# Optimization experiments

Hardware: AMD Instinct MI355X
Metric: run time of the kernel (lower is better)

## Reference

```python
import jax, jax.numpy as jnp
import numpy as np

B, M, E, R, U, I = 4096, 100, 128, 64, 100000, 100000


def setup_inputs() -> dict:
    key = jax.random.key(0)
    ks = jax.random.split(key, 10)
    return {
        "user_id": jax.random.randint(ks[0], (B,), 0, U),
        "item_id_p": jax.random.randint(ks[1], (B,), 0, I),
        "item_id_n": jax.random.randint(ks[2], (B,), 0, I),
        "inter_id": jax.random.randint(ks[3], (B, M), 0, I),
        "user_emb_w": jax.random.normal(ks[4], (U, E), jnp.float32),
        "item_emb_w": jax.random.normal(ks[5], (I, E), jnp.float32),
        "ua_key": jax.random.normal(ks[6], (R, E), jnp.float32),
        "ua_val": jax.random.normal(ks[7], (R, E), jnp.float32),
        "ia_key": jax.random.normal(ks[8], (R, E), jnp.float32),
        "ia_val": jax.random.normal(ks[9], (R, E), jnp.float32),
    }


def _maxnorm_lookup(w, ids, max_norm=1.0, eps=1e-7):
    # torch nn.Embedding(max_norm=1): rows with norm > max_norm are renormalized
    v = w[ids]
    n = jnp.linalg.norm(v, axis=-1, keepdims=True)
    scale = jnp.where(n > max_norm, max_norm / (n + eps), jnp.ones_like(n))
    return v * scale


def _rel_attn(key_w, val_w, mul_feat, attn_feat, inter):
    # w = key*val elementwise (R,E); einsum 'mbj,ij->bmj' sums w over relations
    wsum = jnp.sum(key_w * val_w, axis=0)                 # (E,)
    rel = mul_feat[:, None, :] * inter * wsum             # (B,M,E) rel_vecs
    logits = jnp.einsum("bme,be->bm", rel, attn_feat)      # (B,M)
    attn = jax.nn.softmax(logits, axis=1)
    return jnp.einsum("bm,bme->be", attn, rel)             # (B,E)


def reference(user_id, item_id_p, item_id_n, inter_id,
              user_emb_w, item_emb_w, ua_key, ua_val, ia_key, ia_val):
    u = _maxnorm_lookup(user_emb_w, user_id)
    ip = _maxnorm_lookup(item_emb_w, item_id_p)
    inn = _maxnorm_lookup(item_emb_w, item_id_n)
    inter = _maxnorm_lookup(item_emb_w, inter_id)
    # UserAttention: rel from item*inter, softmax vs user
    # ItemAttention (model_type='plus'): rel from user*inter, softmax vs item
    rel_p = _rel_attn(ua_key, ua_val, ip, u, inter) + _rel_attn(ia_key, ia_val, u, ip, inter)
    rel_n = _rel_attn(ua_key, ua_val, inn, u, inter) + _rel_attn(ia_key, ia_val, u, inn, inter)
    return (u, ip, inn, rel_p, rel_n)
```

## Files before the change

kernel.cpp:

```cpp
#include <hip/hip_runtime.h>
#include <math.h>

#define BB 4096
#define MM 100
#define EE 128
#define RR 64

typedef float v4f __attribute__((ext_vector_type(4)));
typedef float v2f __attribute__((ext_vector_type(2)));

__device__ __forceinline__ v4f ld4v(const float* p) {
    return *reinterpret_cast<const v4f*>(p);
}
__device__ __forceinline__ void st4v(float* p, v4f v) {
    *reinterpret_cast<v4f*>(p) = v;
}
__device__ __forceinline__ float pdot8(v4f a, v4f qa, v4f b, v4f qb) {
    v2f acc = a.xy * qa.xy;
    acc += a.zw * qa.zw;
    acc += b.xy * qb.xy;
    acc += b.zw * qb.zw;
    return acc.x + acc.y;
}
__device__ __forceinline__ v4f v4red(v4f a, int off) {
    a.x += __shfl_xor(a.x, off, 64); a.y += __shfl_xor(a.y, off, 64);
    a.z += __shfl_xor(a.z, off, 64); a.w += __shfl_xor(a.w, off, 64);
    return a;
}
__device__ __forceinline__ v4f relcomb(v4f x1, v4f w1, v4f S1v, float i1,
                                       v4f x2, v4f w2, v4f S2v, float i2) {
    return x1 * w1 * (S1v * i1) + x2 * w2 * (S2v * i2);
}

template<int CTRL>
__device__ __forceinline__ float dpp_add(float x) {
    int y = __builtin_amdgcn_update_dpp(0, __float_as_int(x), CTRL, 0xF, 0xF, true);
    return x + __int_as_float(y);
}
__device__ __forceinline__ float row16_allreduce(float x) {
    x = dpp_add<0x121>(x);
    x = dpp_add<0x122>(x);
    x = dpp_add<0x124>(x);
    x = dpp_add<0x128>(x);
    return x;
}

__global__ __launch_bounds__(512)
void wsum_kernel(const float* __restrict__ ua_key, const float* __restrict__ ua_val,
                 const float* __restrict__ ia_key, const float* __restrict__ ia_val,
                 float* __restrict__ ws) {
    __shared__ float part[4][EE];
    const float* k = (blockIdx.x == 0) ? ua_key : ia_key;
    const float* v = (blockIdx.x == 0) ? ua_val : ia_val;
    int e = threadIdx.x & 127;
    int q = threadIdx.x >> 7;
    float s = 0.f;
    #pragma unroll
    for (int j = 0; j < 16; ++j) {
        int r = q * 16 + j;
        s += k[r * EE + e] * v[r * EE + e];
    }
    part[q][e] = s;
    __syncthreads();
    if (threadIdx.x < EE)
        ws[blockIdx.x * EE + e] = part[0][e] + part[1][e] + part[2][e] + part[3][e];
}

__global__ __launch_bounds__(64)
void hlrm_main(const int* __restrict__ user_id,
               const int* __restrict__ ip_id,
               const int* __restrict__ in_id,
               const int* __restrict__ inter_id,
               const float* __restrict__ user_w,
               const float* __restrict__ item_w,
               const float* __restrict__ ws,
               float* __restrict__ out) {
    __shared__ int sw[MM];

    const int b    = blockIdx.x;
    const int lane = threadIdx.x;
    const int g    = lane >> 4;
    const int hl   = lane & 15;
    const int e0   = hl * 4;

    const int* ib = inter_id + b * MM;
    int sid0 = ib[g], sid1 = ib[4 + g], sid2 = ib[8 + g], sid3 = ib[12 + g];
    if (lane < 50)
        *reinterpret_cast<int2*>(sw + 2 * lane) =
            *reinterpret_cast<const int2*>(ib + 2 * lane);

    int uid = user_id[b], pid = ip_id[b], nid = in_id[b];
    const float* pu = user_w + ((uint)uid << 7);
    const float* pp = item_w + ((uint)pid << 7);
    const float* pn = item_w + ((uint)nid << 7);
    v4f ru_a = ld4v(pu + e0), ru_b = ld4v(pu + e0 + 64);
    v4f rp_a = ld4v(pp + e0), rp_b = ld4v(pp + e0 + 64);
    v4f rn_a = ld4v(pn + e0), rn_b = ld4v(pn + e0 + 64);
    v4f waa = ld4v(ws + e0),       wab = ld4v(ws + e0 + 64);
    v4f wia = ld4v(ws + 128 + e0), wib = ld4v(ws + 192 + e0);

    v4f va0, vb0, va1, vb1, va2, vb2, va3, vb3;
#define LOADT(J) do {                                             \
        const float* pt = item_w + ((uint)sid##J << 7) + e0;      \
        va##J = ld4v(pt);                                         \
        vb##J = ld4v(pt + 64);                                    \
    } while (0)
    LOADT(0); LOADT(1); LOADT(2); LOADT(3);

    float ssu = pdot8(ru_a, ru_a, ru_b, ru_b);
    float ssp = pdot8(rp_a, rp_a, rp_b, rp_b);
    float ssn = pdot8(rn_a, rn_a, rn_b, rn_b);
    ssu = row16_allreduce(ssu);
    ssp = row16_allreduce(ssp);
    ssn = row16_allreduce(ssn);
    float scu = (ssu > 1.f) ? __builtin_amdgcn_rsqf(ssu) : 1.f;
    float scp = (ssp > 1.f) ? __builtin_amdgcn_rsqf(ssp) : 1.f;
    float scn = (ssn > 1.f) ? __builtin_amdgcn_rsqf(ssn) : 1.f;

    float cup = scu * scp, cun = scu * scn;
    v4f qa0 = ru_a * rp_a * waa * cup, qb0 = ru_b * rp_b * wab * cup;
    v4f qa1 = ru_a * rp_a * wia * cup, qb1 = ru_b * rp_b * wib * cup;
    v4f qa2 = ru_a * rn_a * waa * cun, qb2 = ru_b * rn_b * wab * cun;
    v4f qa3 = ru_a * rn_a * wia * cun, qb3 = ru_b * rn_b * wib * cun;

    v4f Sa0 = {0,0,0,0}, Sa1 = {0,0,0,0}, Sa2 = {0,0,0,0}, Sa3 = {0,0,0,0};
    v4f Sb0 = {0,0,0,0}, Sb1 = {0,0,0,0}, Sb2 = {0,0,0,0}, Sb3 = {0,0,0,0};
    float den0 = 0.f, den1 = 0.f, den2 = 0.f, den3 = 0.f;

    sid0 = sw[16 + g]; sid1 = sw[20 + g]; sid2 = sw[24 + g]; sid3 = sw[28 + g];

#define STEP(J) do {                                                        \
        float ss = pdot8(va##J, va##J, vb##J, vb##J);                       \
        float d0 = pdot8(va##J, qa0, vb##J, qb0);                           \
        float d1 = pdot8(va##J, qa1, vb##J, qb1);                           \
        float d2 = pdot8(va##J, qa2, vb##J, qb2);                           \
        float d3 = pdot8(va##J, qa3, vb##J, qb3);                           \
        ss = row16_allreduce(ss);                                           \
        d0 = row16_allreduce(d0); d1 = row16_allreduce(d1);                 \
        d2 = row16_allreduce(d2); d3 = row16_allreduce(d3);                 \
        float sc = (ss > 1.f) ? __builtin_amdgcn_rsqf(ss) : 1.f;            \
        float w0 = __expf(d0 * sc), w1 = __expf(d1 * sc);                   \
        float w2 = __expf(d2 * sc), w3 = __expf(d3 * sc);                   \
        den0 += w0; den1 += w1; den2 += w2; den3 += w3;                     \
        w0 *= sc; w1 *= sc; w2 *= sc; w3 *= sc;                             \
        Sa0 += va##J * w0; Sb0 += vb##J * w0;                               \
        Sa1 += va##J * w1; Sb1 += vb##J * w1;                               \
        Sa2 += va##J * w2; Sb2 += vb##J * w2;                               \
        Sa3 += va##J * w3; Sb3 += vb##J * w3;                               \
    } while (0)

    #pragma unroll 1
    for (int it = 0; it < 5; ++it) {
        STEP(0); LOADT(0);
        STEP(1); LOADT(1);
        STEP(2); LOADT(2);
        STEP(3); LOADT(3);
        if (it < 4) {
            int o = 16 * it + 32 + g;
            sid0 = sw[o]; sid1 = sw[o + 4]; sid2 = sw[o + 8]; sid3 = sw[o + 12];
        }
    }
    sid0 = sw[96 + g];
    STEP(0); LOADT(0);
    STEP(1); STEP(2); STEP(3);
    STEP(0);
#undef STEP
#undef LOADT

    #pragma unroll
    for (int off = 16; off < 64; off <<= 1) {
        Sa0 = v4red(Sa0, off); Sb0 = v4red(Sb0, off);
        Sa1 = v4red(Sa1, off); Sb1 = v4red(Sb1, off);
        Sa2 = v4red(Sa2, off); Sb2 = v4red(Sb2, off);
        Sa3 = v4red(Sa3, off); Sb3 = v4red(Sb3, off);
        den0 += __shfl_xor(den0, off, 64);
        den1 += __shfl_xor(den1, off, 64);
        den2 += __shfl_xor(den2, off, 64);
        den3 += __shfl_xor(den3, off, 64);
    }
    float iD0 = 1.f / den0, iD1 = 1.f / den1, iD2 = 1.f / den2, iD3 = 1.f / den3;

    const float* qu = user_w + ((uint)uid << 7);
    const float* qp = item_w + ((uint)pid << 7);
    const float* qn = item_w + ((uint)nid << 7);
    v4f u_a = ld4v(qu + e0) * scu,      u_b = ld4v(qu + e0 + 64) * scu;
    v4f p_a = ld4v(qp + e0) * scp,      p_b = ld4v(qp + e0 + 64) * scp;
    v4f n_a = ld4v(qn + e0) * scn,      n_b = ld4v(qn + e0 + 64) * scn;
    v4f w0a = ld4v(ws + e0),            w0b = ld4v(ws + e0 + 64);
    v4f w1a = ld4v(ws + 128 + e0),      w1b = ld4v(ws + 192 + e0);

    size_t base = (size_t)b * EE;
    const size_t P = (size_t)BB * EE;
    if (g == 0) {
        v4f ra = relcomb(p_a, w0a, Sa0, iD0, u_a, w1a, Sa1, iD1);
        v4f rb = relcomb(p_b, w0b, Sb0, iD0, u_b, w1b, Sb1, iD1);
        st4v(out + 3 * P + base + e0, ra);
        st4v(out + 3 * P + base + e0 + 64, rb);
    } else if (g == 1) {
        v4f ra = relcomb(n_a, w0a, Sa2, iD2, u_a, w1a, Sa3, iD3);
        v4f rb = relcomb(n_b, w0b, Sb2, iD2, u_b, w1b, Sb3, iD3);
        st4v(out + 4 * P + base + e0, ra);
        st4v(out + 4 * P + base + e0 + 64, rb);
    } else if (g == 2) {
        st4v(out + 0 * P + base + e0, u_a);
        st4v(out + 0 * P + base + e0 + 64, u_b);
        st4v(out + 1 * P + base + e0, p_a);
        st4v(out + 1 * P + base + e0 + 64, p_b);
    } else {
        st4v(out + 2 * P + base + e0, n_a);
        st4v(out + 2 * P + base + e0 + 64, n_b);
    }
}

extern "C" void kernel_launch(void* const* d_in, const int* in_sizes, int n_in,
                              void* d_out, int out_size, void* d_ws, size_t ws_size,
                              hipStream_t stream) {
    const int*   user_id   = (const int*)d_in[0];
    const int*   item_id_p = (const int*)d_in[1];
    const int*   item_id_n = (const int*)d_in[2];
    const int*   inter_id  = (const int*)d_in[3];
    const float* user_w    = (const float*)d_in[4];
    const float* item_w    = (const float*)d_in[5];
    const float* ua_key    = (const float*)d_in[6];
    const float* ua_val    = (const float*)d_in[7];
    const float* ia_key    = (const float*)d_in[8];
    const float* ia_val    = (const float*)d_in[9];
    float* out = (float*)d_out;
    float* ws  = (float*)d_ws;

    wsum_kernel<<<2, 512, 0, stream>>>(ua_key, ua_val, ia_key, ia_val, ws);
    hlrm_main<<<BB, 64, 0, stream>>>(user_id, item_id_p, item_id_n, inter_id,
                                     user_w, item_w, ws, out);
}
```

Measured before the change: 44.18 us.

## Split history rows across two wavefronts per batch with LDS reduction

Each block now runs two wavefronts that share the 100 interaction rows, each handling half (13 steps instead of 25). A padded tail step masks out the invalid rows. Partial softmax numerators and denominators are combined through shared memory after a barrier. The final combine and output stores are rewritten so each of the 128 threads writes one element per output. The aim is to shorten the serial latency chain per batch row and raise the number of wavefronts in flight, at the cost of two barriers and extra LDS traffic.

```diff
diff --git a/kernel.cpp b/kernel.cpp
--- a/kernel.cpp
+++ b/kernel.cpp
@@ -11,9 +11,6 @@
 
 __device__ __forceinline__ v4f ld4v(const float* p) {
     return *reinterpret_cast<const v4f*>(p);
-}
-__device__ __forceinline__ void st4v(float* p, v4f v) {
-    *reinterpret_cast<v4f*>(p) = v;
 }
 __device__ __forceinline__ float pdot8(v4f a, v4f qa, v4f b, v4f qb) {
     v2f acc = a.xy * qa.xy;
@@ -26,10 +23,6 @@
     a.x += __shfl_xor(a.x, off, 64); a.y += __shfl_xor(a.y, off, 64);
     a.z += __shfl_xor(a.z, off, 64); a.w += __shfl_xor(a.w, off, 64);
     return a;
-}
-__device__ __forceinline__ v4f relcomb(v4f x1, v4f w1, v4f S1v, float i1,
-                                       v4f x2, v4f w2, v4f S2v, float i2) {
-    return x1 * w1 * (S1v * i1) + x2 * w2 * (S2v * i2);
 }
 
 template<int CTRL>
@@ -66,7 +59,7 @@
         ws[blockIdx.x * EE + e] = part[0][e] + part[1][e] + part[2][e] + part[3][e];
 }
 
-__global__ __launch_bounds__(64)
+__global__ __launch_bounds__(128)
 void hlrm_main(const int* __restrict__ user_id,
                const int* __restrict__ ip_id,
                const int* __restrict__ in_id,
@@ -75,19 +68,26 @@
                const float* __restrict__ item_w,
                const float* __restrict__ ws,
                float* __restrict__ out) {
-    __shared__ int sw[MM];
+    __shared__ int   sw[104];
+    __shared__ float s_part[2][4][EE];
+    __shared__ float s_den[2][4];
 
     const int b    = blockIdx.x;
-    const int lane = threadIdx.x;
+    const int tid  = threadIdx.x;
+    const int lane = tid & 63;
+    const int w    = tid >> 6;
     const int g    = lane >> 4;
     const int hl   = lane & 15;
     const int e0   = hl * 4;
+    const int idx  = 2 * g + w;
 
     const int* ib = inter_id + b * MM;
-    int sid0 = ib[g], sid1 = ib[4 + g], sid2 = ib[8 + g], sid3 = ib[12 + g];
-    if (lane < 50)
-        *reinterpret_cast<int2*>(sw + 2 * lane) =
-            *reinterpret_cast<const int2*>(ib + 2 * lane);
+    if (tid < 50)
+        *reinterpret_cast<int2*>(sw + 2 * tid) =
+            *reinterpret_cast<const int2*>(ib + 2 * tid);
+    if (tid >= 50 && tid < 52) { sw[2 * tid] = 0; sw[2 * tid + 1] = 0; }
+
+    int sid0 = ib[idx], sid1 = ib[8 + idx], sid2 = ib[16 + idx], sid3 = ib[24 + idx];
 
     int uid = user_id[b], pid = ip_id[b], nid = in_id[b];
     const float* pu = user_w + ((uint)uid << 7);
@@ -127,9 +127,11 @@
     v4f Sb0 = {0,0,0,0}, Sb1 = {0,0,0,0}, Sb2 = {0,0,0,0}, Sb3 = {0,0,0,0};
     float den0 = 0.f, den1 = 0.f, den2 = 0.f, den3 = 0.f;
 
-    sid0 = sw[16 + g]; sid1 = sw[20 + g]; sid2 = sw[24 + g]; sid3 = sw[28 + g];
-
-#define STEP(J) do {                                                        \
+    __syncthreads();
+
+    sid0 = sw[32 + idx]; sid1 = sw[40 + idx]; sid2 = sw[48 + idx]; sid3 = sw[56 + idx];
+
+#define STEP(J, MASKED) do {                                                \
         float ss = pdot8(va##J, va##J, vb##J, vb##J);                       \
         float d0 = pdot8(va##J, qa0, vb##J, qb0);                           \
         float d1 = pdot8(va##J, qa1, vb##J, qb1);                           \
@@ -141,6 +143,7 @@
         float sc = (ss > 1.f) ? __builtin_amdgcn_rsqf(ss) : 1.f;            \
         float w0 = __expf(d0 * sc), w1 = __expf(d1 * sc);                   \
         float w2 = __expf(d2 * sc), w3 = __expf(d3 * sc);                   \
+        if (MASKED && idx >= 4) { w0 = 0.f; w1 = 0.f; w2 = 0.f; w3 = 0.f; } \
         den0 += w0; den1 += w1; den2 += w2; den3 += w3;                     \
         w0 *= sc; w1 *= sc; w2 *= sc; w3 *= sc;                             \
         Sa0 += va##J * w0; Sb0 += vb##J * w0;                               \
@@ -150,20 +153,21 @@
     } while (0)
 
     #pragma unroll 1
-    for (int it = 0; it < 5; ++it) {
-        STEP(0); LOADT(0);
-        STEP(1); LOADT(1);
-        STEP(2); LOADT(2);
-        STEP(3); LOADT(3);
-        if (it < 4) {
-            int o = 16 * it + 32 + g;
-            sid0 = sw[o]; sid1 = sw[o + 4]; sid2 = sw[o + 8]; sid3 = sw[o + 12];
+    for (int it = 0; it < 2; ++it) {
+        STEP(0, 0); LOADT(0);
+        STEP(1, 0); LOADT(1);
+        STEP(2, 0); LOADT(2);
+        STEP(3, 0); LOADT(3);
+        if (it == 0) {
+            sid0 = sw[64 + idx]; sid1 = sw[72 + idx];
+            sid2 = sw[80 + idx]; sid3 = sw[88 + idx];
+        } else {
+            sid0 = sw[96 + idx];
         }
     }
-    sid0 = sw[96 + g];
-    STEP(0); LOADT(0);
-    STEP(1); STEP(2); STEP(3);
-    STEP(0);
+    STEP(0, 0); LOADT(0);
+    STEP(1, 0); STEP(2, 0); STEP(3, 0);
+    STEP(0, 1);
 #undef STEP
 #undef LOADT
 
@@ -178,37 +182,45 @@
         den2 += __shfl_xor(den2, off, 64);
         den3 += __shfl_xor(den3, off, 64);
     }
-    float iD0 = 1.f / den0, iD1 = 1.f / den1, iD2 = 1.f / den2, iD3 = 1.f / den3;
-
-    const float* qu = user_w + ((uint)uid << 7);
-    const float* qp = item_w + ((uint)pid << 7);
-    const float* qn = item_w + ((uint)nid << 7);
-    v4f u_a = ld4v(qu + e0) * scu,      u_b = ld4v(qu + e0 + 64) * scu;
-    v4f p_a = ld4v(qp + e0) * scp,      p_b = ld4v(qp + e0 + 64) * scp;
-    v4f n_a = ld4v(qn + e0) * scn,      n_b = ld4v(qn + e0 + 64) * scn;
-    v4f w0a = ld4v(ws + e0),            w0b = ld4v(ws + e0 + 64);
-    v4f w1a = ld4v(ws + 128 + e0),      w1b = ld4v(ws + 192 + e0);
-
-    size_t base = (size_t)b * EE;
-    const size_t P = (size_t)BB * EE;
     if (g == 0) {
-        v4f ra = relcomb(p_a, w0a, Sa0, iD0, u_a, w1a, Sa1, iD1);
-        v4f rb = relcomb(p_b, w0b, Sb0, iD0, u_b, w1b, Sb1, iD1);
-        st4v(out + 3 * P + base + e0, ra);
-        st4v(out + 3 * P + base + e0 + 64, rb);
-    } else if (g == 1) {
-        v4f ra = relcomb(n_a, w0a, Sa2, iD2, u_a, w1a, Sa3, iD3);
-        v4f rb = relcomb(n_b, w0b, Sb2, iD2, u_b, w1b, Sb3, iD3);
-        st4v(out + 4 * P + base + e0, ra);
-        st4v(out + 4 * P + base + e0 + 64, rb);
-    } else if (g == 2) {
-        st4v(out + 0 * P + base + e0, u_a);
-        st4v(out + 0 * P + base + e0 + 64, u_b);
-        st4v(out + 1 * P + base + e0, p_a);
-        st4v(out + 1 * P + base + e0 + 64, p_b);
-    } else {
-        st4v(out + 2 * P + base + e0, n_a);
-        st4v(out + 2 * P + base + e0 + 64, n_b);
+        *reinterpret_cast<v4f*>(&s_part[w][0][e0]) = Sa0;
+        *reinterpret_cast<v4f*>(&s_part[w][0][e0 + 64]) = Sb0;
+        *reinterpret_cast<v4f*>(&s_part[w][1][e0]) = Sa1;
+        *reinterpret_cast<v4f*>(&s_part[w][1][e0 + 64]) = Sb1;
+        *reinterpret_cast<v4f*>(&s_part[w][2][e0]) = Sa2;
+        *reinterpret_cast<v4f*>(&s_part[w][2][e0 + 64]) = Sb2;
+        *reinterpret_cast<v4f*>(&s_part[w][3][e0]) = Sa3;
+        *reinterpret_cast<v4f*>(&s_part[w][3][e0 + 64]) = Sb3;
+        if (hl == 0) {
+            s_den[w][0] = den0; s_den[w][1] = den1;
+            s_den[w][2] = den2; s_den[w][3] = den3;
+        }
+    }
+    __syncthreads();
+
+    {
+        int e = tid;
+        float iD0 = 1.f / (s_den[0][0] + s_den[1][0]);
+        float iD1 = 1.f / (s_den[0][1] + s_den[1][1]);
+        float iD2 = 1.f / (s_den[0][2] + s_den[1][2]);
+        float iD3 = 1.f / (s_den[0][3] + s_den[1][3]);
+        float S0e = (s_part[0][0][e] + s_part[1][0][e]) * iD0;
+        float S1e = (s_part[0][1][e] + s_part[1][1][e]) * iD1;
+        float S2e = (s_part[0][2][e] + s_part[1][2][e]) * iD2;
+        float S3e = (s_part[0][3][e] + s_part[1][3][e]) * iD3;
+        float u  = user_w[((uint)uid << 7) + e] * scu;
+        float ip = item_w[((uint)pid << 7) + e] * scp;
+        float nn = item_w[((uint)nid << 7) + e] * scn;
+        float wae = ws[e], wie = ws[EE + e];
+        float relp = ip * wae * S0e + u * wie * S1e;
+        float reln = nn * wae * S2e + u * wie * S3e;
+        size_t base = (size_t)b * EE + e;
+        const size_t P = (size_t)BB * EE;
+        out[0 * P + base] = u;
+        out[1 * P + base] = ip;
+        out[2 * P + base] = nn;
+        out[3 * P + base] = relp;
+        out[4 * P + base] = reln;
     }
 }
 
@@ -229,6 +241,6 @@
     float* ws  = (float*)d_ws;
 
     wsum_kernel<<<2, 512, 0, stream>>>(ua_key, ua_val, ia_key, ia_val, ws);
-    hlrm_main<<<BB, 64, 0, stream>>>(user_id, item_id_p, item_id_n, inter_id,
-                                     user_w, item_w, ws, out);
-}
+    hlrm_main<<<BB, 128, 0, stream>>>(user_id, item_id_p, item_id_n, inter_id,
+                                      user_w, item_w, ws, out);
+}
```

New measurement: 47.32 us. 7.1% more time.
